# Optimization experiments

Measured on AMD Instinct MI355X. Metric: run time of the kernel, lower is better.

Reference implementation:

```python
import jax, jax.numpy as jnp
import numpy as np

EMBED_DIM = 768
HEAD_SIZE = 64

def setup_inputs() -> dict:
    key = jax.random.key(0)
    k1, k2, k3, k4 = jax.random.split(key, 4)
    x = jax.random.normal(k1, (4, 4096, EMBED_DIM), dtype=jnp.float32)
    # nn.Linear(E, H, bias=False) weights, stored as [E, H] for y = x @ W
    scale = 1.0 / np.sqrt(EMBED_DIM)
    Wk = jax.random.uniform(k2, (EMBED_DIM, HEAD_SIZE), jnp.float32, -scale, scale)
    Wq = jax.random.uniform(k3, (EMBED_DIM, HEAD_SIZE), jnp.float32, -scale, scale)
    Wv = jax.random.uniform(k4, (EMBED_DIM, HEAD_SIZE), jnp.float32, -scale, scale)
    return {"x": x, "Wk": Wk, "Wq": Wq, "Wv": Wv}

def reference(x, Wk, Wq, Wv):
    # x: [B, S, E]
    E = x.shape[2]
    K = jnp.einsum("bse,eh->bsh", x, Wk)  # [B, S, H]
    Q = jnp.einsum("bse,eh->bsh", x, Wq)
    V = jnp.einsum("bse,eh->bsh", x, Wv)
    # NOTE: original scales by embedding_dim**0.5, not head_size**0.5
    A = jnp.einsum("bqh,bkh->bqk", Q, K) / jnp.sqrt(jnp.asarray(E, x.dtype))
    A = jax.nn.softmax(A, axis=-1)
    # dropout is inference-mode identity
    return jnp.einsum("bqk,bkh->bqh", A, V)
```

## Files before the change

kernel.cpp:

```cpp
#include <hip/hip_runtime.h>

typedef __attribute__((ext_vector_type(8))) short short8;
typedef __attribute__((ext_vector_type(4))) short short4v;
typedef __attribute__((ext_vector_type(4))) float float4v;

__device__ __forceinline__ short f2bf(float f) {
    union { float f; unsigned u; } v; v.f = f;
    return (short)((v.u + 0x7fffu + ((v.u >> 16) & 1u)) >> 16);
}

__device__ __forceinline__ float fast_exp2(float x) {
#if __has_builtin(__builtin_amdgcn_exp2f)
    return __builtin_amdgcn_exp2f(x);
#else
    return exp2f(x);
#endif
}

__global__ void wtrans_kernel(const float* __restrict__ Wk, const float* __restrict__ Wq,
                              const float* __restrict__ Wv, short* __restrict__ Wt3T) {
    int idx = blockIdx.x * 256 + threadIdx.x;
    int p = idx / 12288;
    int rem = idx - p * 12288;
    int kstep = rem / 512;
    int r2 = rem - kstep * 512;
    int lane = r2 >> 3, i = r2 & 7;
    int quad = lane >> 4, l16 = lane & 15;
    int j = p >> 2, nt = p & 3;
    int n = nt * 16 + l16;
    int k = kstep * 32 + quad * 8 + i;
    const float* W = (j == 0) ? Wq : (j == 1 ? Wk : Wv);
    float scale = (j == 0) ? 0.05205877f : 1.0f;
    Wt3T[idx] = f2bf(W[k * 64 + n] * scale);
}

__global__ __launch_bounds__(256) void proj_kernel(
    const float* __restrict__ x, const short* __restrict__ Wt3T,
    short* __restrict__ Qs, short* __restrict__ Kb, short* __restrict__ Vtr)
{
    __shared__ alignas(16) short sm[16 * 72];
    const int tid = threadIdx.x;
    const int wave = tid >> 6, lane = tid & 63, quad = lane >> 4, l16 = lane & 15;
    const int m0 = blockIdx.x * 16;
    const int p0 = wave * 3;
    const float* xr = x + (size_t)(m0 + l16) * 768 + quad * 8;
    const short* wt0 = Wt3T + (size_t)(p0 * 24) * 512 + lane * 8;

    float4 X[3][2];
    short8 Wf[3][3];
#pragma unroll
    for (int s = 0; s < 2; ++s) {
        X[s][0] = *(const float4*)(xr + s * 32);
        X[s][1] = *(const float4*)(xr + s * 32 + 4);
#pragma unroll
        for (int t = 0; t < 3; ++t)
            Wf[s][t] = *(const short8*)(wt0 + t * 12288 + s * 512);
    }

    float4v acc[3];
#pragma unroll
    for (int t = 0; t < 3; ++t) acc[t] = (float4v){0.f, 0.f, 0.f, 0.f};

#pragma unroll
    for (int it = 0; it < 24; ++it) {
        const int cur = it % 3, nxt = (it + 2) % 3;
        if (it < 22) {
            X[nxt][0] = *(const float4*)(xr + (it + 2) * 32);
            X[nxt][1] = *(const float4*)(xr + (it + 2) * 32 + 4);
#pragma unroll
            for (int t = 0; t < 3; ++t)
                Wf[nxt][t] = *(const short8*)(wt0 + t * 12288 + (it + 2) * 512);
        }
        short8 a;
        a[0] = f2bf(X[cur][0].x); a[1] = f2bf(X[cur][0].y);
        a[2] = f2bf(X[cur][0].z); a[3] = f2bf(X[cur][0].w);
        a[4] = f2bf(X[cur][1].x); a[5] = f2bf(X[cur][1].y);
        a[6] = f2bf(X[cur][1].z); a[7] = f2bf(X[cur][1].w);
#pragma unroll
        for (int t = 0; t < 3; ++t)
            acc[t] = __builtin_amdgcn_mfma_f32_16x16x32_bf16(a, Wf[cur][t], acc[t], 0, 0, 0);
    }

#pragma unroll
    for (int t = 0; t < 3; ++t) {
        const int p = p0 + t, j = p >> 2, nt = p & 3;
        if (j < 2) {
            short* dst = (j == 0) ? Qs : Kb;
#pragma unroll
            for (int r = 0; r < 4; ++r)
                dst[(size_t)(m0 + quad * 4 + r) * 64 + nt * 16 + l16] = f2bf(acc[t][r]);
        } else {
#pragma unroll
            for (int r = 0; r < 4; ++r)
                sm[(quad * 4 + r) * 72 + nt * 16 + l16] = f2bf(acc[t][r]);
        }
    }
    __syncthreads();
    {
        const int h = tid >> 2, si = (tid & 3) * 4;
        const int b = m0 >> 12, s0 = m0 & 4095;
        short4v tmp;
#pragma unroll
        for (int i = 0; i < 4; ++i) tmp[i] = sm[(si + i) * 72 + h];
        *(short4v*)(Vtr + (size_t)(b * 64 + h) * 4096 + s0 + si) = tmp;
    }
}

__global__ __launch_bounds__(256, 4) void attn_kernel(
    const short* __restrict__ Qs, const short* __restrict__ Kb, const short* __restrict__ Vt,
    float* __restrict__ Opart, float* __restrict__ Ll, int kv_len)
{
    __shared__ alignas(16) short Kl[64 * 72];
    __shared__ alignas(16) short Vl[64 * 72];
    __shared__ alignas(16) short Pl[4 * 32 * 72];

    const int tid = threadIdx.x;
    const int wave = tid >> 6, lane = tid & 63, quad = lane >> 4, l16 = lane & 15;
    const int qt = blockIdx.x, b = blockIdx.y, sp = blockIdx.z;
    const int q0 = qt * 128;
    const int bS = b * 4096;
    const int kv0 = sp * kv_len;

    short8 qa[2][2];
#pragma unroll
    for (int mt = 0; mt < 2; ++mt)
#pragma unroll
        for (int ks = 0; ks < 2; ++ks)
            qa[mt][ks] = *(const short8*)(Qs + (size_t)(bS + q0 + wave * 32 + mt * 16 + l16) * 64 + ks * 32 + quad * 8);

    float4v o[2][4];
    float rs[2][4];
#pragma unroll
    for (int mt = 0; mt < 2; ++mt)
#pragma unroll
        for (int nt = 0; nt < 4; ++nt) o[mt][nt] = (float4v){0.f, 0.f, 0.f, 0.f};
#pragma unroll
    for (int mt = 0; mt < 2; ++mt)
#pragma unroll
        for (int r = 0; r < 4; ++r) rs[mt][r] = 0.f;

    const int sr = tid >> 2, sc = (tid & 3) * 16;
    short* plw = &Pl[wave * 2304];

    for (int kt = 0; kt < kv_len; kt += 64) {
        const int kvg = kv0 + kt;
        __syncthreads();
        {
            const short* src = Kb + (size_t)(bS + kvg + sr) * 64 + sc;
            *(short8*)&Kl[sr * 72 + sc]     = *(const short8*)src;
            *(short8*)&Kl[sr * 72 + sc + 8] = *(const short8*)(src + 8);
            const short* vs = Vt + (size_t)(b * 64 + sr) * 4096 + kvg + sc;
            *(short8*)&Vl[sr * 72 + sc]     = *(const short8*)vs;
            *(short8*)&Vl[sr * 72 + sc + 8] = *(const short8*)(vs + 8);
        }
        __syncthreads();

        float4v s[2][4];
#pragma unroll
        for (int nt = 0; nt < 4; ++nt) {
            short8 b0 = *(const short8*)&Kl[(nt * 16 + l16) * 72 + quad * 8];
            short8 b1 = *(const short8*)&Kl[(nt * 16 + l16) * 72 + 32 + quad * 8];
#pragma unroll
            for (int mt = 0; mt < 2; ++mt) {
                float4v a0 = (float4v){0.f, 0.f, 0.f, 0.f};
                a0 = __builtin_amdgcn_mfma_f32_16x16x32_bf16(qa[mt][0], b0, a0, 0, 0, 0);
                a0 = __builtin_amdgcn_mfma_f32_16x16x32_bf16(qa[mt][1], b1, a0, 0, 0, 0);
                s[mt][nt] = a0;
            }
        }

#pragma unroll
        for (int mt = 0; mt < 2; ++mt)
#pragma unroll
            for (int nt = 0; nt < 4; ++nt)
#pragma unroll
                for (int r = 0; r < 4; ++r) {
                    float p = fast_exp2(s[mt][nt][r]);
                    rs[mt][r] += p;
                    plw[(mt * 16 + quad * 4 + r) * 72 + nt * 16 + l16] = f2bf(p);
                }

#pragma unroll
        for (int ks = 0; ks < 2; ++ks) {
            short8 bf[4];
#pragma unroll
            for (int nt = 0; nt < 4; ++nt)
                bf[nt] = *(const short8*)&Vl[(nt * 16 + l16) * 72 + ks * 32 + quad * 8];
#pragma unroll
            for (int mt = 0; mt < 2; ++mt) {
                short8 af = *(const short8*)&plw[(mt * 16 + l16) * 72 + ks * 32 + quad * 8];
#pragma unroll
                for (int nt = 0; nt < 4; ++nt)
                    o[mt][nt] = __builtin_amdgcn_mfma_f32_16x16x32_bf16(af, bf[nt], o[mt][nt], 0, 0, 0);
            }
        }
    }

#pragma unroll
    for (int mt = 0; mt < 2; ++mt)
#pragma unroll
        for (int r = 0; r < 4; ++r) {
#pragma unroll
            for (int off = 8; off >= 1; off >>= 1)
                rs[mt][r] += __shfl_xor(rs[mt][r], off);
        }

#pragma unroll
    for (int mt = 0; mt < 2; ++mt) {
#pragma unroll
        for (int nt = 0; nt < 4; ++nt)
#pragma unroll
            for (int r = 0; r < 4; ++r) {
                int qb = q0 + wave * 32 + mt * 16 + quad * 4 + r;
                Opart[((size_t)sp * 16384 + bS + qb) * 64 + nt * 16 + l16] = o[mt][nt][r];
            }
        if (l16 == 0) {
#pragma unroll
            for (int r = 0; r < 4; ++r) {
                int qb = q0 + wave * 32 + mt * 16 + quad * 4 + r;
                Ll[(size_t)sp * 16384 + bS + qb] = rs[mt][r];
            }
        }
    }
}

__global__ void combine_kernel(const float* __restrict__ Opart, const float* __restrict__ Ll,
                               float* __restrict__ out, int nsplit) {
    int idx = blockIdx.x * 256 + threadIdx.x;
    int q = idx >> 6;
    float den = 0.f, num = 0.f;
    for (int s = 0; s < nsplit; ++s) {
        den += Ll[s * 16384 + q];
        num += Opart[(size_t)s * 1048576 + idx];
    }
    out[idx] = num / den;
}

extern "C" void kernel_launch(void* const* d_in, const int* in_sizes, int n_in,
                              void* d_out, int out_size, void* d_ws, size_t ws_size,
                              hipStream_t stream) {
    const float* x  = (const float*)d_in[0];
    const float* Wk = (const float*)d_in[1];
    const float* Wq = (const float*)d_in[2];
    const float* Wv = (const float*)d_in[3];
    float* out = (float*)d_out;

    char* w = (char*)d_ws;
    size_t off = 0;
    auto take = [&](size_t bytes) -> void* {
        void* p = w + off;
        off = (off + bytes + 255) & ~(size_t)255;
        return p;
    };
    short* Qs  = (short*)take((size_t)16384 * 64 * 2);
    short* Kb  = (short*)take((size_t)16384 * 64 * 2);
    short* Vt  = (short*)take((size_t)16384 * 64 * 2);
    short* Wt3 = (short*)take((size_t)3 * 64 * 768 * 2);

    size_t base = off;
    int nsplit = 8;
    while (nsplit > 1) {
        size_t need = base + (((size_t)nsplit * 16384 * 4 + 255) & ~(size_t)255)
                      + (size_t)nsplit * 16384 * 64 * 4 + 512;
        if (need <= ws_size) break;
        nsplit >>= 1;
    }
    float* Ll    = (float*)take((size_t)nsplit * 16384 * 4);
    float* Opart = (float*)take((size_t)nsplit * 16384 * 64 * 4);

    wtrans_kernel<<<576, 256, 0, stream>>>(Wk, Wq, Wv, Wt3);
    proj_kernel<<<1024, 256, 0, stream>>>(x, Wt3, Qs, Kb, Vt);
    dim3 ag(32, 4, nsplit);
    attn_kernel<<<ag, 256, 0, stream>>>(Qs, Kb, Vt, Opart, Ll, 4096 / nsplit);
    combine_kernel<<<4096, 256, 0, stream>>>(Opart, Ll, out, nsplit);
}
```

Measured before the change: 154.1 us.

## Share bf16-converted x tile across waves via LDS in projection kernel

Before, each of the four waves loaded and converted the same 16-row x slice to bf16 in its own registers. Now each thread loads one float2, converts it once, and writes it into a triple-buffered LDS tile that all waves read as MFMA A operands. Weight prefetch depth drops from two steps to one, and launch_bounds now asks for 4 blocks per CU. This removes redundant global x loads and conversions, but adds a __syncthreads per K step and LDS traffic.

```diff
diff --git a/kernel.cpp b/kernel.cpp
--- a/kernel.cpp
+++ b/kernel.cpp
@@ -34,51 +34,58 @@
     Wt3T[idx] = f2bf(W[k * 64 + n] * scale);
 }
 
-__global__ __launch_bounds__(256) void proj_kernel(
+__global__ __launch_bounds__(256, 4) void proj_kernel(
     const float* __restrict__ x, const short* __restrict__ Wt3T,
     short* __restrict__ Qs, short* __restrict__ Kb, short* __restrict__ Vtr)
 {
+    __shared__ alignas(16) int Abuf[3][256];
     __shared__ alignas(16) short sm[16 * 72];
     const int tid = threadIdx.x;
     const int wave = tid >> 6, lane = tid & 63, quad = lane >> 4, l16 = lane & 15;
     const int m0 = blockIdx.x * 16;
     const int p0 = wave * 3;
-    const float* xr = x + (size_t)(m0 + l16) * 768 + quad * 8;
+
+    const int xrow = tid >> 4, xcol = (tid & 15) * 2;
+    const float* xp = x + (size_t)(m0 + xrow) * 768 + xcol;
+    const int aidx = xrow * 16 + (tid & 15);
     const short* wt0 = Wt3T + (size_t)(p0 * 24) * 512 + lane * 8;
 
-    float4 X[3][2];
-    short8 Wf[3][3];
-#pragma unroll
-    for (int s = 0; s < 2; ++s) {
-        X[s][0] = *(const float4*)(xr + s * 32);
-        X[s][1] = *(const float4*)(xr + s * 32 + 4);
-#pragma unroll
-        for (int t = 0; t < 3; ++t)
-            Wf[s][t] = *(const short8*)(wt0 + t * 12288 + s * 512);
-    }
-
     float4v acc[3];
 #pragma unroll
     for (int t = 0; t < 3; ++t) acc[t] = (float4v){0.f, 0.f, 0.f, 0.f};
 
+    {
+        float2 u = *(const float2*)xp;
+        Abuf[0][aidx] = ((unsigned short)f2bf(u.x)) | ((unsigned)f2bf(u.y) << 16);
+    }
+    short8 Wc0 = *(const short8*)(wt0);
+    short8 Wc1 = *(const short8*)(wt0 + 12288);
+    short8 Wc2 = *(const short8*)(wt0 + 24576);
+    float2 Xn = *(const float2*)(xp + 32);
+    __syncthreads();
+
 #pragma unroll
     for (int it = 0; it < 24; ++it) {
-        const int cur = it % 3, nxt = (it + 2) % 3;
-        if (it < 22) {
-            X[nxt][0] = *(const float4*)(xr + (it + 2) * 32);
-            X[nxt][1] = *(const float4*)(xr + (it + 2) * 32 + 4);
-#pragma unroll
-            for (int t = 0; t < 3; ++t)
-                Wf[nxt][t] = *(const short8*)(wt0 + t * 12288 + (it + 2) * 512);
-        }
-        short8 a;
-        a[0] = f2bf(X[cur][0].x); a[1] = f2bf(X[cur][0].y);
-        a[2] = f2bf(X[cur][0].z); a[3] = f2bf(X[cur][0].w);
-        a[4] = f2bf(X[cur][1].x); a[5] = f2bf(X[cur][1].y);
-        a[6] = f2bf(X[cur][1].z); a[7] = f2bf(X[cur][1].w);
-#pragma unroll
-        for (int t = 0; t < 3; ++t)
-            acc[t] = __builtin_amdgcn_mfma_f32_16x16x32_bf16(a, Wf[cur][t], acc[t], 0, 0, 0);
+        short8 Wn0, Wn1, Wn2;
+        float2 Xn2;
+        if (it < 23) {
+            const short* wn = wt0 + (it + 1) * 512;
+            Wn0 = *(const short8*)(wn);
+            Wn1 = *(const short8*)(wn + 12288);
+            Wn2 = *(const short8*)(wn + 24576);
+        }
+        if (it < 22) Xn2 = *(const float2*)(xp + (it + 2) * 32);
+
+        short8 a = *(const short8*)((const short*)Abuf[it % 3] + l16 * 32 + quad * 8);
+        acc[0] = __builtin_amdgcn_mfma_f32_16x16x32_bf16(a, Wc0, acc[0], 0, 0, 0);
+        acc[1] = __builtin_amdgcn_mfma_f32_16x16x32_bf16(a, Wc1, acc[1], 0, 0, 0);
+        acc[2] = __builtin_amdgcn_mfma_f32_16x16x32_bf16(a, Wc2, acc[2], 0, 0, 0);
+
+        if (it < 23)
+            Abuf[(it + 1) % 3][aidx] = ((unsigned short)f2bf(Xn.x)) | ((unsigned)f2bf(Xn.y) << 16);
+        Xn = Xn2;
+        Wc0 = Wn0; Wc1 = Wn1; Wc2 = Wn2;
+        __syncthreads();
     }
 
 #pragma unroll
```

Result: faster. 144.2 us (-6.4%).

## Stage x tile in LDS for projection and merge split-KV via atomics

Applied to the files above, without the earlier changes.

The projection kernel now loads the 16x768 x tile cooperatively into LDS as packed bf16, then runs the MFMA loop from LDS with weights read directly. The split-KV partial outputs and row sums are accumulated with atomicAdd into the output and a row-sum buffer, replacing the Opart workspace and the combine pass with a simple normalize kernel. Rounding is simplified to round-half-up for P and x. This cuts the partial-buffer write and read traffic, but adds two memsets, atomic contention, and nondeterministic summation order.

```diff
diff --git a/kernel.cpp b/kernel.cpp
--- a/kernel.cpp
+++ b/kernel.cpp
@@ -3,10 +3,15 @@
 typedef __attribute__((ext_vector_type(8))) short short8;
 typedef __attribute__((ext_vector_type(4))) short short4v;
 typedef __attribute__((ext_vector_type(4))) float float4v;
+typedef __attribute__((ext_vector_type(2))) int int2v;
 
 __device__ __forceinline__ short f2bf(float f) {
     union { float f; unsigned u; } v; v.f = f;
     return (short)((v.u + 0x7fffu + ((v.u >> 16) & 1u)) >> 16);
+}
+__device__ __forceinline__ int pack2(float a, float b) {
+    union { float f; unsigned u; } x, y; x.f = a; y.f = b;
+    return (int)(((x.u + 0x8000u) >> 16) | ((y.u + 0x8000u) & 0xFFFF0000u));
 }
 
 __device__ __forceinline__ float fast_exp2(float x) {
@@ -34,53 +39,50 @@
     Wt3T[idx] = f2bf(W[k * 64 + n] * scale);
 }
 
-__global__ __launch_bounds__(256) void proj_kernel(
+__global__ __launch_bounds__(256, 3) void proj_kernel(
     const float* __restrict__ x, const short* __restrict__ Wt3T,
     short* __restrict__ Qs, short* __restrict__ Kb, short* __restrict__ Vtr)
 {
-    __shared__ alignas(16) short sm[16 * 72];
+    __shared__ alignas(16) short As[24 * 512];
     const int tid = threadIdx.x;
     const int wave = tid >> 6, lane = tid & 63, quad = lane >> 4, l16 = lane & 15;
     const int m0 = blockIdx.x * 16;
     const int p0 = wave * 3;
-    const float* xr = x + (size_t)(m0 + l16) * 768 + quad * 8;
-    const short* wt0 = Wt3T + (size_t)(p0 * 24) * 512 + lane * 8;
-
-    float4 X[3][2];
-    short8 Wf[3][3];
-#pragma unroll
-    for (int s = 0; s < 2; ++s) {
-        X[s][0] = *(const float4*)(xr + s * 32);
-        X[s][1] = *(const float4*)(xr + s * 32 + 4);
-#pragma unroll
-        for (int t = 0; t < 3; ++t)
-            Wf[s][t] = *(const short8*)(wt0 + t * 12288 + s * 512);
-    }
-
-    float4v acc[3];
-#pragma unroll
-    for (int t = 0; t < 3; ++t) acc[t] = (float4v){0.f, 0.f, 0.f, 0.f};
+
+    {
+        const int r = tid >> 4, c16 = tid & 15;
+        const float* xp = x + (size_t)(m0 + r) * 768 + c16 * 4;
+        float4 v[12];
+#pragma unroll
+        for (int ch = 0; ch < 12; ++ch) v[ch] = *(const float4*)(xp + ch * 64);
+#pragma unroll
+        for (int ch = 0; ch < 12; ++ch) {
+            const int cb = c16 * 4 + ch * 64;
+            const int sidx = (cb >> 5) * 512 + ((((cb >> 3) & 3) * 16 + r) << 3) + (cb & 7);
+            *(int2v*)&As[sidx] = (int2v){pack2(v[ch].x, v[ch].y), pack2(v[ch].z, v[ch].w)};
+        }
+    }
+    __syncthreads();
+
+    const short* wp0 = Wt3T + (size_t)(p0 + 0) * 12288 + lane * 8;
+    const short* wp1 = Wt3T + (size_t)(p0 + 1) * 12288 + lane * 8;
+    const short* wp2 = Wt3T + (size_t)(p0 + 2) * 12288 + lane * 8;
+
+    float4v acc0 = (float4v){0.f, 0.f, 0.f, 0.f};
+    float4v acc1 = acc0, acc2 = acc0;
 
 #pragma unroll
     for (int it = 0; it < 24; ++it) {
-        const int cur = it % 3, nxt = (it + 2) % 3;
-        if (it < 22) {
-            X[nxt][0] = *(const float4*)(xr + (it + 2) * 32);
-            X[nxt][1] = *(const float4*)(xr + (it + 2) * 32 + 4);
-#pragma unroll
-            for (int t = 0; t < 3; ++t)
-                Wf[nxt][t] = *(const short8*)(wt0 + t * 12288 + (it + 2) * 512);
-        }
-        short8 a;
-        a[0] = f2bf(X[cur][0].x); a[1] = f2bf(X[cur][0].y);
-        a[2] = f2bf(X[cur][0].z); a[3] = f2bf(X[cur][0].w);
-        a[4] = f2bf(X[cur][1].x); a[5] = f2bf(X[cur][1].y);
-        a[6] = f2bf(X[cur][1].z); a[7] = f2bf(X[cur][1].w);
-#pragma unroll
-        for (int t = 0; t < 3; ++t)
-            acc[t] = __builtin_amdgcn_mfma_f32_16x16x32_bf16(a, Wf[cur][t], acc[t], 0, 0, 0);
-    }
-
+        short8 a = *(const short8*)&As[it * 512 + lane * 8];
+        short8 w0 = *(const short8*)(wp0 + it * 512);
+        short8 w1 = *(const short8*)(wp1 + it * 512);
+        short8 w2 = *(const short8*)(wp2 + it * 512);
+        acc0 = __builtin_amdgcn_mfma_f32_16x16x32_bf16(a, w0, acc0, 0, 0, 0);
+        acc1 = __builtin_amdgcn_mfma_f32_16x16x32_bf16(a, w1, acc1, 0, 0, 0);
+        acc2 = __builtin_amdgcn_mfma_f32_16x16x32_bf16(a, w2, acc2, 0, 0, 0);
+    }
+
+    float4v accs[3] = {acc0, acc1, acc2};
 #pragma unroll
     for (int t = 0; t < 3; ++t) {
         const int p = p0 + t, j = p >> 2, nt = p & 3;
@@ -88,12 +90,18 @@
             short* dst = (j == 0) ? Qs : Kb;
 #pragma unroll
             for (int r = 0; r < 4; ++r)
-                dst[(size_t)(m0 + quad * 4 + r) * 64 + nt * 16 + l16] = f2bf(acc[t][r]);
-        } else {
+                dst[(size_t)(m0 + quad * 4 + r) * 64 + nt * 16 + l16] = f2bf(accs[t][r]);
+        }
+    }
+    __syncthreads();
+    short* sm = As;
+#pragma unroll
+    for (int t = 0; t < 3; ++t) {
+        const int p = p0 + t, nt = p & 3;
+        if ((p >> 2) == 2)
 #pragma unroll
             for (int r = 0; r < 4; ++r)
-                sm[(quad * 4 + r) * 72 + nt * 16 + l16] = f2bf(acc[t][r]);
-        }
+                sm[(quad * 4 + r) * 72 + nt * 16 + l16] = f2bf(accs[t][r]);
     }
     __syncthreads();
     {
@@ -108,7 +116,7 @@
 
 __global__ __launch_bounds__(256, 4) void attn_kernel(
     const short* __restrict__ Qs, const short* __restrict__ Kb, const short* __restrict__ Vt,
-    float* __restrict__ Opart, float* __restrict__ Ll, int kv_len)
+    float* __restrict__ out, float* __restrict__ Lsum, int kv_len)
 {
     __shared__ alignas(16) short Kl[64 * 72];
     __shared__ alignas(16) short Vl[64 * 72];
@@ -177,7 +185,8 @@
                 for (int r = 0; r < 4; ++r) {
                     float p = fast_exp2(s[mt][nt][r]);
                     rs[mt][r] += p;
-                    plw[(mt * 16 + quad * 4 + r) * 72 + nt * 16 + l16] = f2bf(p);
+                    plw[(mt * 16 + quad * 4 + r) * 72 + nt * 16 + l16] =
+                        (short)((__float_as_uint(p) + 0x8000u) >> 16);
                 }
 
 #pragma unroll
@@ -212,28 +221,21 @@
 #pragma unroll
             for (int r = 0; r < 4; ++r) {
                 int qb = q0 + wave * 32 + mt * 16 + quad * 4 + r;
-                Opart[((size_t)sp * 16384 + bS + qb) * 64 + nt * 16 + l16] = o[mt][nt][r];
+                atomicAdd(&out[(size_t)(bS + qb) * 64 + nt * 16 + l16], o[mt][nt][r]);
             }
         if (l16 == 0) {
 #pragma unroll
             for (int r = 0; r < 4; ++r) {
                 int qb = q0 + wave * 32 + mt * 16 + quad * 4 + r;
-                Ll[(size_t)sp * 16384 + bS + qb] = rs[mt][r];
-            }
-        }
-    }
-}
-
-__global__ void combine_kernel(const float* __restrict__ Opart, const float* __restrict__ Ll,
-                               float* __restrict__ out, int nsplit) {
+                atomicAdd(&Lsum[bS + qb], rs[mt][r]);
+            }
+        }
+    }
+}
+
+__global__ void normalize_kernel(float* __restrict__ out, const float* __restrict__ Lsum) {
     int idx = blockIdx.x * 256 + threadIdx.x;
-    int q = idx >> 6;
-    float den = 0.f, num = 0.f;
-    for (int s = 0; s < nsplit; ++s) {
-        den += Ll[s * 16384 + q];
-        num += Opart[(size_t)s * 1048576 + idx];
-    }
-    out[idx] = num / den;
+    out[idx] /= Lsum[idx >> 6];
 }
 
 extern "C" void kernel_launch(void* const* d_in, const int* in_sizes, int n_in,
@@ -252,25 +254,19 @@
         off = (off + bytes + 255) & ~(size_t)255;
         return p;
     };
-    short* Qs  = (short*)take((size_t)16384 * 64 * 2);
-    short* Kb  = (short*)take((size_t)16384 * 64 * 2);
-    short* Vt  = (short*)take((size_t)16384 * 64 * 2);
-    short* Wt3 = (short*)take((size_t)3 * 64 * 768 * 2);
-
-    size_t base = off;
-    int nsplit = 8;
-    while (nsplit > 1) {
-        size_t need = base + (((size_t)nsplit * 16384 * 4 + 255) & ~(size_t)255)
-                      + (size_t)nsplit * 16384 * 64 * 4 + 512;
-        if (need <= ws_size) break;
-        nsplit >>= 1;
-    }
-    float* Ll    = (float*)take((size_t)nsplit * 16384 * 4);
-    float* Opart = (float*)take((size_t)nsplit * 16384 * 64 * 4);
+    short* Qs   = (short*)take((size_t)16384 * 64 * 2);
+    short* Kb   = (short*)take((size_t)16384 * 64 * 2);
+    short* Vt   = (short*)take((size_t)16384 * 64 * 2);
+    short* Wt3  = (short*)take((size_t)3 * 64 * 768 * 2);
+    float* Lsum = (float*)take((size_t)16384 * 4);
+
+    hipMemsetAsync(out, 0, (size_t)out_size * sizeof(float), stream);
+    hipMemsetAsync(Lsum, 0, (size_t)16384 * 4, stream);
 
     wtrans_kernel<<<576, 256, 0, stream>>>(Wk, Wq, Wv, Wt3);
     proj_kernel<<<1024, 256, 0, stream>>>(x, Wt3, Qs, Kb, Vt);
+    const int nsplit = 8;
     dim3 ag(32, 4, nsplit);
-    attn_kernel<<<ag, 256, 0, stream>>>(Qs, Kb, Vt, Opart, Ll, 4096 / nsplit);
-    combine_kernel<<<4096, 256, 0, stream>>>(Opart, Ll, out, nsplit);
-}
+    attn_kernel<<<ag, 256, 0, stream>>>(Qs, Kb, Vt, out, Lsum, 4096 / nsplit);
+    normalize_kernel<<<4096, 256, 0, stream>>>(out, Lsum);
+}
```

Result: no change. 153.0 us (-0.7%).
